# Kernel tuning notes

Hardware: AMD Instinct MI355X
Metric: run time of the kernel (lower is better)

## Reference

```python
import jax, jax.numpy as jnp
import numpy as np

D_MODEL = 128
DEPTH = 4
LN_EPS = 1e-5


def _ssm(x, Wi, A, Wo):
    # x: [B, L, D]; Wi: [3D, D]; A: [D]; Wo: [D, D]
    z = jnp.einsum('bld,ed->ble', x, Wi)          # [B, L, 3D]
    u, i, o = jnp.split(z, 3, axis=-1)
    iu = jax.nn.sigmoid(i) * jnp.tanh(u)          # gated input, [B, L, D]
    og = jax.nn.sigmoid(o)                        # output gate
    a = jnp.minimum(jnp.exp(A), 0.999)            # decay, [D]

    def step(s, c):
        s = a * s + c
        return s, s

    s0 = jnp.zeros((x.shape[0], x.shape[2]), x.dtype)
    _, S = jax.lax.scan(step, s0, jnp.swapaxes(iu, 0, 1))  # [L, B, D]
    y = og * jnp.swapaxes(S, 0, 1)                # [B, L, D]
    return jnp.einsum('bld,ed->ble', y, Wo)


def _scan_2d(x, Wi, A, Wo):
    # x: [N, D, H, W] -> four directional 1D scans, averaged
    N, D, H, W = x.shape
    xh = jnp.transpose(x, (0, 2, 3, 1))           # [N, H, W, D]
    lr = _ssm(xh.reshape(N * H, W, D), Wi, A, Wo).reshape(N, H, W, D)
    rl = _ssm(jnp.flip(xh, 2).reshape(N * H, W, D), Wi, A, Wo).reshape(N, H, W, D)
    rl = jnp.flip(rl, 2)
    xw = jnp.transpose(x, (0, 3, 2, 1))           # [N, W, H, D]
    ud = _ssm(xw.reshape(N * W, H, D), Wi, A, Wo).reshape(N, W, H, D)
    du = _ssm(jnp.flip(xw, 2).reshape(N * W, H, D), Wi, A, Wo).reshape(N, W, H, D)
    du = jnp.flip(du, 2)
    y = (lr + rl + jnp.transpose(ud, (0, 2, 1, 3)) + jnp.transpose(du, (0, 2, 1, 3))) / 4
    return jnp.transpose(y, (0, 3, 1, 2))         # [N, D, H, W]


def setup_inputs() -> dict:
    key = jax.random.key(0)
    ks = jax.random.split(key, 8)
    D = D_MODEL
    lin = 1.0 / np.sqrt(D)
    tok = jax.random.normal(ks[0], (8, 16, D, 32, 32), jnp.float32)
    s_inp = jax.random.normal(ks[1], (DEPTH, 3 * D, D), jnp.float32) * lin
    s_A = jax.random.normal(ks[2], (DEPTH, D), jnp.float32) * -0.1
    s_out = jax.random.normal(ks[3], (DEPTH, D, D), jnp.float32) * lin
    t_inp = jax.random.normal(ks[4], (DEPTH, 3 * D, D), jnp.float32) * lin
    t_A = jax.random.normal(ks[5], (DEPTH, D), jnp.float32) * -0.1
    t_out = jax.random.normal(ks[6], (DEPTH, D, D), jnp.float32) * lin
    ln_g = jnp.ones((D,), jnp.float32)
    ln_b = jnp.zeros((D,), jnp.float32)
    return {"tok": tok, "s_inp": s_inp, "s_A": s_A, "s_out": s_out,
            "t_inp": t_inp, "t_A": t_A, "t_out": t_out,
            "ln_g": ln_g, "ln_b": ln_b}


def reference(tok, s_inp, s_A, s_out, t_inp, t_A, t_out, ln_g, ln_b):
    B, T, D, h, w = tok.shape
    x = tok
    for l in range(DEPTH):
        xs = x.reshape(B * T, D, h, w)
        xs = _scan_2d(xs, s_inp[l], s_A[l], s_out[l]).reshape(B, T, D, h, w)
        xt = jnp.transpose(xs, (0, 3, 4, 1, 2)).reshape(B * h * w, T, D)
        xt = _ssm(xt, t_inp[l], t_A[l], t_out[l]).reshape(B, h, w, T, D)
        x = x + jnp.transpose(xt, (0, 3, 4, 1, 2))
    xn = jnp.transpose(x, (0, 1, 3, 4, 2))        # [B,T,h,w,D]
    mu = jnp.mean(xn, axis=-1, keepdims=True)
    var = jnp.var(xn, axis=-1, keepdims=True)
    xn = (xn - mu) / jnp.sqrt(var + LN_EPS) * ln_g + ln_b
    return jnp.transpose(xn, (0, 1, 4, 2, 3))     # [B,T,D,h,w]
```

## Files before the change

### kernel.cpp

```cpp
#include <hip/hip_runtime.h>
#include <hip/hip_bf16.h>
#include <math.h>

#define D_MODEL 128
#define HW      1024
#define DEPTH   4
#define NIMG    128
#define B_      8
#define T_      16
#define LN_EPSF 1e-5f

typedef short  short8 __attribute__((ext_vector_type(8)));
typedef float  f32x4  __attribute__((ext_vector_type(4)));

__device__ __forceinline__ float sig_(float x) { return 1.0f / (1.0f + __expf(-x)); }
__device__ __forceinline__ float tanh_(float x) { return 2.0f * sig_(2.0f * x) - 1.0f; }

__device__ __forceinline__ ushort f2b(float f) {
    __hip_bfloat16 h = __float2bfloat16(f);
    return *reinterpret_cast<ushort*>(&h);
}
__device__ __forceinline__ float b2f(ushort u) {
    __hip_bfloat16 h = *reinterpret_cast<__hip_bfloat16*>(&u);
    return __bfloat162float(h);
}

__global__ __launch_bounds__(256) void wconv_kernel(
    const float* __restrict__ src, ushort* __restrict__ dst, int n)
{
    int i = blockIdx.x * 256 + threadIdx.x;
    if (i < n) dst[i] = f2b(src[i]);
}

template <typename InT>
__global__ __launch_bounds__(256, 2) void gates_mfma_kernel(
    const InT* __restrict__ in, const ushort* __restrict__ Wi,
    ushort* __restrict__ iu, ushort* __restrict__ og)
{
    __shared__ ushort Xs[64][136];
    const int n   = blockIdx.x >> 4;
    const int q0  = (blockIdx.x & 15) << 6;
    const int tid = threadIdx.x;
    const size_t nbase = (size_t)n * (D_MODEL * HW);

    {
        const InT* inb = in + nbase + q0;
        const int q   = tid & 63;
        const int dh0 = tid >> 6;
        for (int it = 0; it < 4; ++it) {
            const int dh = dh0 + it * 4;
            short8 pk;
            #pragma unroll
            for (int j = 0; j < 8; ++j) {
                float v;
                if constexpr (sizeof(InT) == 4) v = ((const float*)inb)[(size_t)(dh * 8 + j) * HW + q];
                else                            v = b2f(((const ushort*)inb)[(size_t)(dh * 8 + j) * HW + q]);
                pk[j] = (short)f2b(v);
            }
            *reinterpret_cast<short8*>(&Xs[q][dh * 8]) = pk;
        }
    }
    __syncthreads();

    const int lane = tid & 63;
    const int wv   = tid >> 6;
    const int grp  = lane >> 4;
    const int lrow = lane & 15;
    const int ch0  = wv * 32;

    f32x4 aU[2][4], aI[2][4], aO[2][4];
    #pragma unroll
    for (int rt = 0; rt < 2; ++rt)
        #pragma unroll
        for (int ct = 0; ct < 4; ++ct) { aU[rt][ct] = (f32x4)0.f; aI[rt][ct] = (f32x4)0.f; aO[rt][ct] = (f32x4)0.f; }

    #pragma unroll
    for (int kk = 0; kk < 4; ++kk) {
        const int kb = kk * 32 + grp * 8;
        short8 wu[2], wi[2], wo[2], xb[4];
        #pragma unroll
        for (int rt = 0; rt < 2; ++rt) {
            const int e = ch0 + rt * 16 + lrow;
            wu[rt] = *reinterpret_cast<const short8*>(Wi + (size_t)e * D_MODEL + kb);
            wi[rt] = *reinterpret_cast<const short8*>(Wi + (size_t)(e + 128) * D_MODEL + kb);
            wo[rt] = *reinterpret_cast<const short8*>(Wi + (size_t)(e + 256) * D_MODEL + kb);
        }
        #pragma unroll
        for (int ct = 0; ct < 4; ++ct)
            xb[ct] = *reinterpret_cast<const short8*>(&Xs[ct * 16 + lrow][kb]);
        #pragma unroll
        for (int rt = 0; rt < 2; ++rt)
            #pragma unroll
            for (int ct = 0; ct < 4; ++ct) {
                aU[rt][ct] = __builtin_amdgcn_mfma_f32_16x16x32_bf16(wu[rt], xb[ct], aU[rt][ct], 0, 0, 0);
                aI[rt][ct] = __builtin_amdgcn_mfma_f32_16x16x32_bf16(wi[rt], xb[ct], aI[rt][ct], 0, 0, 0);
                aO[rt][ct] = __builtin_amdgcn_mfma_f32_16x16x32_bf16(wo[rt], xb[ct], aO[rt][ct], 0, 0, 0);
            }
    }

    #pragma unroll
    for (int rt = 0; rt < 2; ++rt)
        #pragma unroll
        for (int ct = 0; ct < 4; ++ct)
            #pragma unroll
            for (int i = 0; i < 4; ++i) {
                const int c = ch0 + rt * 16 + grp * 4 + i;
                const int q = q0 + ct * 16 + lrow;
                const size_t idx = nbase + (size_t)c * HW + q;
                iu[idx] = f2b(sig_(aI[rt][ct][i]) * tanh_(aU[rt][ct][i]));
                og[idx] = f2b(sig_(aO[rt][ct][i]));
            }
}

template <typename OutT, bool RES>
__global__ __launch_bounds__(256, 2) void outgemm_mfma_kernel(
    const ushort* __restrict__ S, const ushort* __restrict__ og,
    const ushort* __restrict__ Wo, const float* __restrict__ resid,
    OutT* __restrict__ out, float scale)
{
    __shared__ ushort Gs[64][136];
    const int n   = blockIdx.x >> 4;
    const int q0  = (blockIdx.x & 15) << 6;
    const int tid = threadIdx.x;
    const size_t nbase = (size_t)n * (D_MODEL * HW);

    {
        const ushort* Sb = S  + nbase + q0;
        const ushort* Ob = og + nbase + q0;
        const int q   = tid & 63;
        const int dh0 = tid >> 6;
        for (int it = 0; it < 4; ++it) {
            const int dh = dh0 + it * 4;
            short8 pk;
            #pragma unroll
            for (int j = 0; j < 8; ++j) {
                const size_t o = (size_t)(dh * 8 + j) * HW + q;
                pk[j] = (short)f2b(b2f(Ob[o]) * b2f(Sb[o]) * scale);
            }
            *reinterpret_cast<short8*>(&Gs[q][dh * 8]) = pk;
        }
    }
    __syncthreads();

    const int lane = tid & 63;
    const int wv   = tid >> 6;
    const int grp  = lane >> 4;
    const int lrow = lane & 15;
    const int ch0  = wv * 32;

    f32x4 acc[2][4];
    #pragma unroll
    for (int rt = 0; rt < 2; ++rt)
        #pragma unroll
        for (int ct = 0; ct < 4; ++ct) acc[rt][ct] = (f32x4)0.f;

    #pragma unroll
    for (int kk = 0; kk < 4; ++kk) {
        const int kb = kk * 32 + grp * 8;
        short8 wf[2], xb[4];
        #pragma unroll
        for (int rt = 0; rt < 2; ++rt)
            wf[rt] = *reinterpret_cast<const short8*>(Wo + (size_t)(ch0 + rt * 16 + lrow) * D_MODEL + kb);
        #pragma unroll
        for (int ct = 0; ct < 4; ++ct)
            xb[ct] = *reinterpret_cast<const short8*>(&Gs[ct * 16 + lrow][kb]);
        #pragma unroll
        for (int rt = 0; rt < 2; ++rt)
            #pragma unroll
            for (int ct = 0; ct < 4; ++ct)
                acc[rt][ct] = __builtin_amdgcn_mfma_f32_16x16x32_bf16(wf[rt], xb[ct], acc[rt][ct], 0, 0, 0);
    }

    #pragma unroll
    for (int rt = 0; rt < 2; ++rt)
        #pragma unroll
        for (int ct = 0; ct < 4; ++ct)
            #pragma unroll
            for (int i = 0; i < 4; ++i) {
                const int e = ch0 + rt * 16 + grp * 4 + i;
                const int q = q0 + ct * 16 + lrow;
                const size_t idx = nbase + (size_t)e * HW + q;
                float v = acc[rt][ct][i];
                if constexpr (RES) v += resid[idx];
                if constexpr (sizeof(OutT) == 2) out[idx] = (OutT)f2b(v);
                else                             out[idx] = (OutT)v;
            }
}

__global__ __launch_bounds__(128) void scan2d_kernel(
    ushort* __restrict__ buf, const float* __restrict__ Avec)
{
    __shared__ float L[4][32][33];
    __shared__ float S[4][32][33];
    const int pl = threadIdx.x >> 5;
    const int r  = threadIdx.x & 31;
    const int plane = blockIdx.x * 4 + pl;
    const int d = plane & (D_MODEL - 1);
    ushort* base = buf + (size_t)plane * HW;
    const float a = fminf(__expf(Avec[d]), 0.999f);

    for (int k = 0; k < 32; ++k) L[pl][k][r] = b2f(base[k * 32 + r]);
    __syncthreads();

    {
        float acc[32];
        float s = 0.f;
        #pragma unroll
        for (int j = 0; j < 32; ++j) { s = fmaf(a, s, L[pl][r][j]); acc[j] = s; }
        s = 0.f;
        #pragma unroll
        for (int j = 31; j >= 0; --j) { s = fmaf(a, s, L[pl][r][j]); acc[j] += s; }
        #pragma unroll
        for (int j = 0; j < 32; ++j) S[pl][r][j] = acc[j];
    }
    __syncthreads();
    {
        float s = 0.f;
        #pragma unroll
        for (int i = 0; i < 32; ++i) { s = fmaf(a, s, L[pl][i][r]); S[pl][i][r] += s; }
        s = 0.f;
        #pragma unroll
        for (int i = 31; i >= 0; --i) { s = fmaf(a, s, L[pl][i][r]); S[pl][i][r] += s; }
    }
    __syncthreads();
    for (int k = 0; k < 32; ++k) base[k * 32 + r] = f2b(S[pl][k][r]);
}

__global__ __launch_bounds__(256) void tscan_kernel(
    ushort* __restrict__ buf, const float* __restrict__ Avec)
{
    const int idx = blockIdx.x * 256 + threadIdx.x;
    if (idx >= B_ * D_MODEL * HW) return;
    const int q = idx & (HW - 1);
    const int rest = idx >> 10;
    const int d = rest & (D_MODEL - 1);
    const int b = rest >> 7;
    const float a = fminf(__expf(Avec[d]), 0.999f);
    size_t base = (size_t)b * (T_ * D_MODEL * HW) + (size_t)d * HW + q;
    float s = 0.f;
    for (int t = 0; t < T_; ++t) {
        const size_t id2 = base + (size_t)t * (D_MODEL * HW);
        s = fmaf(a, s, b2f(buf[id2]));
        buf[id2] = f2b(s);
    }
}

__global__ __launch_bounds__(256) void ln_kernel(
    float* __restrict__ X, const float* __restrict__ g, const float* __restrict__ b)
{
    const int p = blockIdx.x * 256 + threadIdx.x;
    if (p >= NIMG * HW) return;
    const int q = p & (HW - 1);
    const int n = p >> 10;
    const size_t base = (size_t)n * (D_MODEL * HW) + q;
    float sum = 0.f, sumsq = 0.f;
    for (int d = 0; d < D_MODEL; ++d) {
        const float x = X[base + (size_t)d * HW];
        sum += x; sumsq += x * x;
    }
    const float mean = sum * (1.f / D_MODEL);
    const float var  = sumsq * (1.f / D_MODEL) - mean * mean;
    const float rstd = rsqrtf(var + LN_EPSF);
    for (int d = 0; d < D_MODEL; ++d) {
        const size_t idx = base + (size_t)d * HW;
        X[idx] = (X[idx] - mean) * rstd * g[d] + b[d];
    }
}

extern "C" void kernel_launch(void* const* d_in, const int* in_sizes, int n_in,
                              void* d_out, int out_size, void* d_ws, size_t ws_size,
                              hipStream_t stream) {
    const float* tok   = (const float*)d_in[0];
    const float* s_inp = (const float*)d_in[1];
    const float* s_A   = (const float*)d_in[2];
    const float* s_out = (const float*)d_in[3];
    const float* t_inp = (const float*)d_in[4];
    const float* t_A   = (const float*)d_in[5];
    const float* t_out = (const float*)d_in[6];
    const float* ln_g  = (const float*)d_in[7];
    const float* ln_b  = (const float*)d_in[8];

    float*  X    = (float*)d_out;
    ushort* Abuf = (ushort*)d_ws;
    ushort* Bbuf = Abuf + (size_t)16777216;
    ushort* Wbf  = Bbuf + (size_t)16777216;
    ushort* sWiB = Wbf;
    ushort* sWoB = Wbf + 196608;
    ushort* tWiB = Wbf + 262144;
    ushort* tWoB = Wbf + 458752;

    const dim3 blk256(256), blk128(128);

    wconv_kernel<<<768, blk256, 0, stream>>>(s_inp, sWiB, 196608);
    wconv_kernel<<<256, blk256, 0, stream>>>(s_out, sWoB, 65536);
    wconv_kernel<<<768, blk256, 0, stream>>>(t_inp, tWiB, 196608);
    wconv_kernel<<<256, blk256, 0, stream>>>(t_out, tWoB, 65536);

    for (int l = 0; l < DEPTH; ++l) {
        const float* xin = (l == 0) ? tok : X;

        gates_mfma_kernel<float><<<2048, blk256, 0, stream>>>(
            xin, sWiB + (size_t)l * 49152, Abuf, Bbuf);
        scan2d_kernel<<<4096, blk128, 0, stream>>>(Abuf, s_A + (size_t)l * 128);
        outgemm_mfma_kernel<ushort, false><<<2048, blk256, 0, stream>>>(
            Abuf, Bbuf, sWoB + (size_t)l * 16384, nullptr, Bbuf, 0.25f);

        gates_mfma_kernel<ushort><<<2048, blk256, 0, stream>>>(
            Bbuf, tWiB + (size_t)l * 49152, Abuf, Bbuf);
        tscan_kernel<<<4096, blk256, 0, stream>>>(Abuf, t_A + (size_t)l * 128);
        outgemm_mfma_kernel<float, true><<<2048, blk256, 0, stream>>>(
            Abuf, Bbuf, tWoB + (size_t)l * 16384, xin, X, 1.0f);
    }
    ln_kernel<<<512, blk256, 0, stream>>>(X, ln_g, ln_b);
}
```

Baseline: 750.7 us.

## Fuse output GEMM with next gate GEMM and vectorize stores and tscan

Fuses each output projection with the following input-gate projection in one kernel, staging the projected activations in LDS so they never round-trip through global memory. Swaps the MFMA operand order so accumulator rows map to spatial positions, which allows 4-wide vector stores for gates and the fp32 residual path. The temporal scan now processes two positions per thread with paired loads. The layer-0 spatial gates kernel is hoisted out of the loop, and fusedB produces the next layer's spatial gates. Trade-offs are higher register pressure and in-place Abuf/Bbuf reads and writes within the fused kernels, which rely on each block touching only its own tile.

```diff
diff --git a/kernel.cpp b/kernel.cpp
--- a/kernel.cpp
+++ b/kernel.cpp
@@ -10,12 +10,13 @@
 #define T_      16
 #define LN_EPSF 1e-5f
 
-typedef short  short8 __attribute__((ext_vector_type(8)));
-typedef float  f32x4  __attribute__((ext_vector_type(4)));
+typedef short  s8  __attribute__((ext_vector_type(8)));
+typedef ushort us4 __attribute__((ext_vector_type(4)));
+typedef ushort us2 __attribute__((ext_vector_type(2)));
+typedef float  f4  __attribute__((ext_vector_type(4)));
 
 __device__ __forceinline__ float sig_(float x) { return 1.0f / (1.0f + __expf(-x)); }
 __device__ __forceinline__ float tanh_(float x) { return 2.0f * sig_(2.0f * x) - 1.0f; }
-
 __device__ __forceinline__ ushort f2b(float f) {
     __hip_bfloat16 h = __float2bfloat16(f);
     return *reinterpret_cast<ushort*>(&h);
@@ -32,9 +33,66 @@
     if (i < n) dst[i] = f2b(src[i]);
 }
 
-template <typename InT>
-__global__ __launch_bounds__(256, 2) void gates_mfma_kernel(
-    const InT* __restrict__ in, const ushort* __restrict__ Wi,
+__device__ __forceinline__ void gates_from_lds(
+    const ushort (*Xs)[136], const ushort* __restrict__ Wi,
+    ushort* __restrict__ iu, ushort* __restrict__ og,
+    size_t nbase, int q0, int tid)
+{
+    const int lane = tid & 63;
+    const int wv   = tid >> 6;
+    const int grp  = lane >> 4;
+    const int lrow = lane & 15;
+    const int ch0  = wv * 32;
+
+    f4 aU[4][2], aI[4][2], aO[4][2];
+    #pragma unroll
+    for (int mt = 0; mt < 4; ++mt)
+        #pragma unroll
+        for (int nt = 0; nt < 2; ++nt) { aU[mt][nt] = (f4)0.f; aI[mt][nt] = (f4)0.f; aO[mt][nt] = (f4)0.f; }
+
+    #pragma unroll
+    for (int kk = 0; kk < 4; ++kk) {
+        const int kb = kk * 32 + grp * 8;
+        s8 xa[4], wu[2], wi[2], wo[2];
+        #pragma unroll
+        for (int mt = 0; mt < 4; ++mt)
+            xa[mt] = *reinterpret_cast<const s8*>(&Xs[mt * 16 + lrow][kb]);
+        #pragma unroll
+        for (int nt = 0; nt < 2; ++nt) {
+            const int e = ch0 + nt * 16 + lrow;
+            wu[nt] = *reinterpret_cast<const s8*>(Wi + (size_t)e * D_MODEL + kb);
+            wi[nt] = *reinterpret_cast<const s8*>(Wi + (size_t)(e + 128) * D_MODEL + kb);
+            wo[nt] = *reinterpret_cast<const s8*>(Wi + (size_t)(e + 256) * D_MODEL + kb);
+        }
+        #pragma unroll
+        for (int mt = 0; mt < 4; ++mt)
+            #pragma unroll
+            for (int nt = 0; nt < 2; ++nt) {
+                aU[mt][nt] = __builtin_amdgcn_mfma_f32_16x16x32_bf16(xa[mt], wu[nt], aU[mt][nt], 0, 0, 0);
+                aI[mt][nt] = __builtin_amdgcn_mfma_f32_16x16x32_bf16(xa[mt], wi[nt], aI[mt][nt], 0, 0, 0);
+                aO[mt][nt] = __builtin_amdgcn_mfma_f32_16x16x32_bf16(xa[mt], wo[nt], aO[mt][nt], 0, 0, 0);
+            }
+    }
+
+    #pragma unroll
+    for (int mt = 0; mt < 4; ++mt)
+        #pragma unroll
+        for (int nt = 0; nt < 2; ++nt) {
+            const int e = ch0 + nt * 16 + lrow;
+            const size_t off = nbase + (size_t)e * HW + q0 + mt * 16 + grp * 4;
+            us4 piu, pog;
+            #pragma unroll
+            for (int i = 0; i < 4; ++i) {
+                piu[i] = f2b(sig_(aI[mt][nt][i]) * tanh_(aU[mt][nt][i]));
+                pog[i] = f2b(sig_(aO[mt][nt][i]));
+            }
+            *reinterpret_cast<us4*>(iu + off) = piu;
+            *reinterpret_cast<us4*>(og + off) = pog;
+        }
+}
+
+__global__ __launch_bounds__(256, 2) void gates_f32_kernel(
+    const float* __restrict__ in, const ushort* __restrict__ Wi,
     ushort* __restrict__ iu, ushort* __restrict__ og)
 {
     __shared__ ushort Xs[64][136];
@@ -44,20 +102,47 @@
     const size_t nbase = (size_t)n * (D_MODEL * HW);
 
     {
-        const InT* inb = in + nbase + q0;
+        const float* inb = in + nbase + q0;
         const int q   = tid & 63;
         const int dh0 = tid >> 6;
         for (int it = 0; it < 4; ++it) {
             const int dh = dh0 + it * 4;
-            short8 pk;
+            s8 pk;
+            #pragma unroll
+            for (int j = 0; j < 8; ++j)
+                pk[j] = (short)f2b(inb[(size_t)(dh * 8 + j) * HW + q]);
+            *reinterpret_cast<s8*>(&Xs[q][dh * 8]) = pk;
+        }
+    }
+    __syncthreads();
+    gates_from_lds(Xs, Wi, iu, og, nbase, q0, tid);
+}
+
+__global__ __launch_bounds__(256, 2) void fusedA_kernel(
+    const ushort* __restrict__ S, const ushort* __restrict__ og_in,
+    const ushort* __restrict__ Wo, const ushort* __restrict__ Wi2,
+    ushort* __restrict__ iu, ushort* __restrict__ og, float scale)
+{
+    __shared__ ushort Gs[64][136];
+    const int n   = blockIdx.x >> 4;
+    const int q0  = (blockIdx.x & 15) << 6;
+    const int tid = threadIdx.x;
+    const size_t nbase = (size_t)n * (D_MODEL * HW);
+
+    {
+        const ushort* Sb = S     + nbase + q0;
+        const ushort* Ob = og_in + nbase + q0;
+        const int q   = tid & 63;
+        const int dh0 = tid >> 6;
+        for (int it = 0; it < 4; ++it) {
+            const int dh = dh0 + it * 4;
+            s8 pk;
             #pragma unroll
             for (int j = 0; j < 8; ++j) {
-                float v;
-                if constexpr (sizeof(InT) == 4) v = ((const float*)inb)[(size_t)(dh * 8 + j) * HW + q];
-                else                            v = b2f(((const ushort*)inb)[(size_t)(dh * 8 + j) * HW + q]);
-                pk[j] = (short)f2b(v);
+                const size_t o = (size_t)(dh * 8 + j) * HW + q;
+                pk[j] = (short)f2b(b2f(Ob[o]) * b2f(Sb[o]) * scale);
             }
-            *reinterpret_cast<short8*>(&Xs[q][dh * 8]) = pk;
+            *reinterpret_cast<s8*>(&Gs[q][dh * 8]) = pk;
         }
     }
     __syncthreads();
@@ -68,55 +153,51 @@
     const int lrow = lane & 15;
     const int ch0  = wv * 32;
 
-    f32x4 aU[2][4], aI[2][4], aO[2][4];
-    #pragma unroll
-    for (int rt = 0; rt < 2; ++rt)
-        #pragma unroll
-        for (int ct = 0; ct < 4; ++ct) { aU[rt][ct] = (f32x4)0.f; aI[rt][ct] = (f32x4)0.f; aO[rt][ct] = (f32x4)0.f; }
+    f4 c1[2][4];
+    #pragma unroll
+    for (int et = 0; et < 2; ++et)
+        #pragma unroll
+        for (int qt = 0; qt < 4; ++qt) c1[et][qt] = (f4)0.f;
 
     #pragma unroll
     for (int kk = 0; kk < 4; ++kk) {
         const int kb = kk * 32 + grp * 8;
-        short8 wu[2], wi[2], wo[2], xb[4];
-        #pragma unroll
-        for (int rt = 0; rt < 2; ++rt) {
-            const int e = ch0 + rt * 16 + lrow;
-            wu[rt] = *reinterpret_cast<const short8*>(Wi + (size_t)e * D_MODEL + kb);
-            wi[rt] = *reinterpret_cast<const short8*>(Wi + (size_t)(e + 128) * D_MODEL + kb);
-            wo[rt] = *reinterpret_cast<const short8*>(Wi + (size_t)(e + 256) * D_MODEL + kb);
-        }
-        #pragma unroll
-        for (int ct = 0; ct < 4; ++ct)
-            xb[ct] = *reinterpret_cast<const short8*>(&Xs[ct * 16 + lrow][kb]);
-        #pragma unroll
-        for (int rt = 0; rt < 2; ++rt)
-            #pragma unroll
-            for (int ct = 0; ct < 4; ++ct) {
-                aU[rt][ct] = __builtin_amdgcn_mfma_f32_16x16x32_bf16(wu[rt], xb[ct], aU[rt][ct], 0, 0, 0);
-                aI[rt][ct] = __builtin_amdgcn_mfma_f32_16x16x32_bf16(wi[rt], xb[ct], aI[rt][ct], 0, 0, 0);
-                aO[rt][ct] = __builtin_amdgcn_mfma_f32_16x16x32_bf16(wo[rt], xb[ct], aO[rt][ct], 0, 0, 0);
-            }
-    }
-
-    #pragma unroll
-    for (int rt = 0; rt < 2; ++rt)
-        #pragma unroll
-        for (int ct = 0; ct < 4; ++ct)
-            #pragma unroll
-            for (int i = 0; i < 4; ++i) {
-                const int c = ch0 + rt * 16 + grp * 4 + i;
-                const int q = q0 + ct * 16 + lrow;
-                const size_t idx = nbase + (size_t)c * HW + q;
-                iu[idx] = f2b(sig_(aI[rt][ct][i]) * tanh_(aU[rt][ct][i]));
-                og[idx] = f2b(sig_(aO[rt][ct][i]));
-            }
-}
-
-template <typename OutT, bool RES>
-__global__ __launch_bounds__(256, 2) void outgemm_mfma_kernel(
-    const ushort* __restrict__ S, const ushort* __restrict__ og,
+        s8 wf[2], xg[4];
+        #pragma unroll
+        for (int et = 0; et < 2; ++et)
+            wf[et] = *reinterpret_cast<const s8*>(Wo + (size_t)(ch0 + et * 16 + lrow) * D_MODEL + kb);
+        #pragma unroll
+        for (int qt = 0; qt < 4; ++qt)
+            xg[qt] = *reinterpret_cast<const s8*>(&Gs[qt * 16 + lrow][kb]);
+        #pragma unroll
+        for (int et = 0; et < 2; ++et)
+            #pragma unroll
+            for (int qt = 0; qt < 4; ++qt)
+                c1[et][qt] = __builtin_amdgcn_mfma_f32_16x16x32_bf16(wf[et], xg[qt], c1[et][qt], 0, 0, 0);
+    }
+    __syncthreads();
+
+    #pragma unroll
+    for (int et = 0; et < 2; ++et)
+        #pragma unroll
+        for (int qt = 0; qt < 4; ++qt) {
+            const int q = qt * 16 + lrow;
+            us4 pk;
+            #pragma unroll
+            for (int i = 0; i < 4; ++i) pk[i] = f2b(c1[et][qt][i]);
+            *reinterpret_cast<us4*>(&Gs[q][ch0 + et * 16 + grp * 4]) = pk;
+        }
+    __syncthreads();
+
+    gates_from_lds(Gs, Wi2, iu, og, nbase, q0, tid);
+}
+
+template <bool GATES>
+__global__ __launch_bounds__(256, 2) void fusedB_kernel(
+    const ushort* __restrict__ S, const ushort* __restrict__ og_in,
     const ushort* __restrict__ Wo, const float* __restrict__ resid,
-    OutT* __restrict__ out, float scale)
+    float* __restrict__ X, const ushort* __restrict__ Wi2,
+    ushort* __restrict__ iu, ushort* __restrict__ og)
 {
     __shared__ ushort Gs[64][136];
     const int n   = blockIdx.x >> 4;
@@ -125,19 +206,19 @@
     const size_t nbase = (size_t)n * (D_MODEL * HW);
 
     {
-        const ushort* Sb = S  + nbase + q0;
-        const ushort* Ob = og + nbase + q0;
+        const ushort* Sb = S     + nbase + q0;
+        const ushort* Ob = og_in + nbase + q0;
         const int q   = tid & 63;
         const int dh0 = tid >> 6;
         for (int it = 0; it < 4; ++it) {
             const int dh = dh0 + it * 4;
-            short8 pk;
+            s8 pk;
             #pragma unroll
             for (int j = 0; j < 8; ++j) {
                 const size_t o = (size_t)(dh * 8 + j) * HW + q;
-                pk[j] = (short)f2b(b2f(Ob[o]) * b2f(Sb[o]) * scale);
+                pk[j] = (short)f2b(b2f(Ob[o]) * b2f(Sb[o]));
             }
-            *reinterpret_cast<short8*>(&Gs[q][dh * 8]) = pk;
+            *reinterpret_cast<s8*>(&Gs[q][dh * 8]) = pk;
         }
     }
     __syncthreads();
@@ -148,43 +229,52 @@
     const int lrow = lane & 15;
     const int ch0  = wv * 32;
 
-    f32x4 acc[2][4];
-    #pragma unroll
-    for (int rt = 0; rt < 2; ++rt)
-        #pragma unroll
-        for (int ct = 0; ct < 4; ++ct) acc[rt][ct] = (f32x4)0.f;
+    f4 c1[4][2];
+    #pragma unroll
+    for (int mt = 0; mt < 4; ++mt)
+        #pragma unroll
+        for (int nt = 0; nt < 2; ++nt) c1[mt][nt] = (f4)0.f;
 
     #pragma unroll
     for (int kk = 0; kk < 4; ++kk) {
         const int kb = kk * 32 + grp * 8;
-        short8 wf[2], xb[4];
-        #pragma unroll
-        for (int rt = 0; rt < 2; ++rt)
-            wf[rt] = *reinterpret_cast<const short8*>(Wo + (size_t)(ch0 + rt * 16 + lrow) * D_MODEL + kb);
-        #pragma unroll
-        for (int ct = 0; ct < 4; ++ct)
-            xb[ct] = *reinterpret_cast<const short8*>(&Gs[ct * 16 + lrow][kb]);
-        #pragma unroll
-        for (int rt = 0; rt < 2; ++rt)
-            #pragma unroll
-            for (int ct = 0; ct < 4; ++ct)
-                acc[rt][ct] = __builtin_amdgcn_mfma_f32_16x16x32_bf16(wf[rt], xb[ct], acc[rt][ct], 0, 0, 0);
-    }
-
-    #pragma unroll
-    for (int rt = 0; rt < 2; ++rt)
-        #pragma unroll
-        for (int ct = 0; ct < 4; ++ct)
-            #pragma unroll
-            for (int i = 0; i < 4; ++i) {
-                const int e = ch0 + rt * 16 + grp * 4 + i;
-                const int q = q0 + ct * 16 + lrow;
-                const size_t idx = nbase + (size_t)e * HW + q;
-                float v = acc[rt][ct][i];
-                if constexpr (RES) v += resid[idx];
-                if constexpr (sizeof(OutT) == 2) out[idx] = (OutT)f2b(v);
-                else                             out[idx] = (OutT)v;
+        s8 xg[4], wf[2];
+        #pragma unroll
+        for (int mt = 0; mt < 4; ++mt)
+            xg[mt] = *reinterpret_cast<const s8*>(&Gs[mt * 16 + lrow][kb]);
+        #pragma unroll
+        for (int nt = 0; nt < 2; ++nt)
+            wf[nt] = *reinterpret_cast<const s8*>(Wo + (size_t)(ch0 + nt * 16 + lrow) * D_MODEL + kb);
+        #pragma unroll
+        for (int mt = 0; mt < 4; ++mt)
+            #pragma unroll
+            for (int nt = 0; nt < 2; ++nt)
+                c1[mt][nt] = __builtin_amdgcn_mfma_f32_16x16x32_bf16(xg[mt], wf[nt], c1[mt][nt], 0, 0, 0);
+    }
+    __syncthreads();
+
+    #pragma unroll
+    for (int mt = 0; mt < 4; ++mt)
+        #pragma unroll
+        for (int nt = 0; nt < 2; ++nt) {
+            const int e    = ch0 + nt * 16 + lrow;
+            const int qloc = mt * 16 + grp * 4;
+            const size_t off = nbase + (size_t)e * HW + q0 + qloc;
+            f4 r = *reinterpret_cast<const f4*>(resid + off);
+            f4 v;
+            #pragma unroll
+            for (int i = 0; i < 4; ++i) v[i] = c1[mt][nt][i] + r[i];
+            *reinterpret_cast<f4*>(X + off) = v;
+            if constexpr (GATES) {
+                #pragma unroll
+                for (int i = 0; i < 4; ++i) Gs[qloc + i][e] = f2b(v[i]);
             }
+        }
+
+    if constexpr (GATES) {
+        __syncthreads();
+        gates_from_lds(Gs, Wi2, iu, og, nbase, q0, tid);
+    }
 }
 
 __global__ __launch_bounds__(128) void scan2d_kernel(
@@ -230,18 +320,19 @@
     ushort* __restrict__ buf, const float* __restrict__ Avec)
 {
     const int idx = blockIdx.x * 256 + threadIdx.x;
-    if (idx >= B_ * D_MODEL * HW) return;
-    const int q = idx & (HW - 1);
-    const int rest = idx >> 10;
-    const int d = rest & (D_MODEL - 1);
-    const int b = rest >> 7;
+    const int qh = idx & 511;
+    const int d  = (idx >> 9) & 127;
+    const int b  = idx >> 16;
     const float a = fminf(__expf(Avec[d]), 0.999f);
-    size_t base = (size_t)b * (T_ * D_MODEL * HW) + (size_t)d * HW + q;
-    float s = 0.f;
+    size_t base = (size_t)b * (T_ * D_MODEL * HW) + (size_t)d * HW + qh * 2;
+    float s0 = 0.f, s1 = 0.f;
     for (int t = 0; t < T_; ++t) {
-        const size_t id2 = base + (size_t)t * (D_MODEL * HW);
-        s = fmaf(a, s, b2f(buf[id2]));
-        buf[id2] = f2b(s);
+        ushort* p = buf + base + (size_t)t * (D_MODEL * HW);
+        us2 v = *reinterpret_cast<us2*>(p);
+        s0 = fmaf(a, s0, b2f(v[0]));
+        s1 = fmaf(a, s1, b2f(v[1]));
+        us2 w; w[0] = f2b(s0); w[1] = f2b(s1);
+        *reinterpret_cast<us2*>(p) = w;
     }
 }
 
@@ -296,20 +387,26 @@
     wconv_kernel<<<768, blk256, 0, stream>>>(t_inp, tWiB, 196608);
     wconv_kernel<<<256, blk256, 0, stream>>>(t_out, tWoB, 65536);
 
+    gates_f32_kernel<<<2048, blk256, 0, stream>>>(tok, sWiB, Abuf, Bbuf);
+
     for (int l = 0; l < DEPTH; ++l) {
         const float* xin = (l == 0) ? tok : X;
 
-        gates_mfma_kernel<float><<<2048, blk256, 0, stream>>>(
-            xin, sWiB + (size_t)l * 49152, Abuf, Bbuf);
         scan2d_kernel<<<4096, blk128, 0, stream>>>(Abuf, s_A + (size_t)l * 128);
-        outgemm_mfma_kernel<ushort, false><<<2048, blk256, 0, stream>>>(
-            Abuf, Bbuf, sWoB + (size_t)l * 16384, nullptr, Bbuf, 0.25f);
-
-        gates_mfma_kernel<ushort><<<2048, blk256, 0, stream>>>(
-            Bbuf, tWiB + (size_t)l * 49152, Abuf, Bbuf);
-        tscan_kernel<<<4096, blk256, 0, stream>>>(Abuf, t_A + (size_t)l * 128);
-        outgemm_mfma_kernel<float, true><<<2048, blk256, 0, stream>>>(
-            Abuf, Bbuf, tWoB + (size_t)l * 16384, xin, X, 1.0f);
+        fusedA_kernel<<<2048, blk256, 0, stream>>>(
+            Abuf, Bbuf, sWoB + (size_t)l * 16384, tWiB + (size_t)l * 49152,
+            Abuf, Bbuf, 0.25f);
+        tscan_kernel<<<2048, blk256, 0, stream>>>(Abuf, t_A + (size_t)l * 128);
+
+        if (l < DEPTH - 1) {
+            fusedB_kernel<true><<<2048, blk256, 0, stream>>>(
+                Abuf, Bbuf, tWoB + (size_t)l * 16384, xin, X,
+                sWiB + (size_t)(l + 1) * 49152, Abuf, Bbuf);
+        } else {
+            fusedB_kernel<false><<<2048, blk256, 0, stream>>>(
+                Abuf, Bbuf, tWoB + (size_t)l * 16384, xin, X,
+                nullptr, nullptr, nullptr);
+        }
     }
     ln_kernel<<<512, blk256, 0, stream>>>(X, ln_g, ln_b);
 }
```

Measured after the change: 707.2 us. 1.06x faster.
